# Performance work log

Measured on AMD Instinct MI355X. Metric: run time of the kernel, lower is better.

## Reference

```python
import jax, jax.numpy as jnp
import numpy as np

B, T, D = 2, 2048, 1024
H, DH = 16, 64
WINDOW = 256
SCALE = DH ** -0.5


def setup_inputs() -> dict:
    key = jax.random.key(0)
    ks = jax.random.split(key, 5)
    x = jax.random.normal(ks[0], (B, T, D), dtype=jnp.float32)
    # Linear params (y = x @ W + b form)
    w_qkv = jax.random.normal(ks[1], (D, 3 * D), dtype=jnp.float32) * (D ** -0.5)
    b_qkv = jnp.zeros((3 * D,), dtype=jnp.float32)
    w_out = jax.random.normal(ks[2], (D, D), dtype=jnp.float32) * (D ** -0.5)
    b_out = jnp.zeros((D,), dtype=jnp.float32)
    return {"x": x, "w_qkv": w_qkv, "b_qkv": b_qkv, "w_out": w_out, "b_out": b_out}


def reference(x, w_qkv, b_qkv, w_out, b_out):
    Bs, Ts, Ds = x.shape
    qkv = x @ w_qkv + b_qkv  # [B,T,3D]
    q, k, v = jnp.split(qkv, 3, axis=-1)
    # [B,H,T,dh]
    def heads(t):
        return t.reshape(Bs, Ts, H, DH).transpose(0, 2, 1, 3)
    q, k, v = heads(q), heads(k), heads(v)
    scores = jnp.einsum('bhqd,bhkd->bhqk', q, k) * SCALE
    i = jnp.arange(Ts)[:, None]
    j = jnp.arange(Ts)[None, :]
    # allowed: i - WINDOW <= j <= i  (causal + local window)
    allowed = (j <= i) & (j >= i - WINDOW)
    scores = jnp.where(allowed, scores, -jnp.inf)
    attn = jax.nn.softmax(scores, axis=-1)  # dropout is identity in eval
    out = jnp.einsum('bhqk,bhkd->bhqd', attn, v)
    out = out.transpose(0, 2, 1, 3).reshape(Bs, Ts, Ds)
    return out @ w_out + b_out
```

## Files before the change

kernel.cpp:

```cpp
#include <hip/hip_runtime.h>

#define BN 2
#define T_DIM 2048
#define D_DIM 1024
#define H_N 16
#define DH_N 64
#define WIN 256
#define NROWS (BN * T_DIM)
#define KDIM 1024

typedef __attribute__((ext_vector_type(8))) short bf16x8;
typedef __attribute__((ext_vector_type(4))) float f32x4;
typedef __attribute__((ext_vector_type(8))) unsigned short ushort8;
typedef __attribute__((ext_vector_type(4))) unsigned short u16x4;

static __device__ __forceinline__ unsigned short f2bf(float f) {
  unsigned int u = __float_as_uint(f);
  unsigned int r = (u + 0x7FFFu + ((u >> 16) & 1u)) >> 16;
  return (unsigned short)r;
}

static __device__ __forceinline__ void gl_lds16(const void* g, void* l) {
  __builtin_amdgcn_global_load_lds(
      (const __attribute__((address_space(1))) unsigned int*)g,
      (__attribute__((address_space(3))) unsigned int*)l, 16, 0, 0);
}

#define MFMA16(a, b, c) __builtin_amdgcn_mfma_f32_16x16x32_bf16(a, b, c, 0, 0, 0)

__global__ __launch_bounds__(256) void convert_bf(const float* __restrict__ src,
                                                  unsigned short* __restrict__ dst) {
  int i = (blockIdx.x * 256 + threadIdx.x) * 8;
  float4 a = *(const float4*)(src + i);
  float4 b = *(const float4*)(src + i + 4);
  ushort8 o;
  o[0] = f2bf(a.x); o[1] = f2bf(a.y); o[2] = f2bf(a.z); o[3] = f2bf(a.w);
  o[4] = f2bf(b.x); o[5] = f2bf(b.y); o[6] = f2bf(b.z); o[7] = f2bf(b.w);
  *(ushort8*)(dst + i) = o;
}

__global__ __launch_bounds__(256) void convert_t(const float* __restrict__ src,
                                                 unsigned short* __restrict__ dst,
                                                 int R, int C) {
  __shared__ float tile[64][65];
  const int t = threadIdx.x;
  const int bc = blockIdx.x * 64, br = blockIdx.y * 64;
#pragma unroll
  for (int i = 0; i < 16; ++i) {
    int idx = i * 256 + t;
    int r = idx >> 6, c = idx & 63;
    tile[r][c] = src[(size_t)(br + r) * C + bc + c];
  }
  __syncthreads();
#pragma unroll
  for (int i = 0; i < 16; ++i) {
    int idx = i * 256 + t;
    int r = idx >> 6, c = idx & 63;
    dst[(size_t)(bc + r) * R + br + c] = f2bf(tile[c][r]);
  }
}

__global__ __launch_bounds__(512) void gemm_qkv_8p(
    const unsigned short* __restrict__ A, const unsigned short* __restrict__ Bt,
    const float* __restrict__ bias, unsigned short* __restrict__ qo,
    unsigned short* __restrict__ ko, unsigned short* __restrict__ vto) {
  __shared__ unsigned short As[2][256 * 64];
  __shared__ unsigned short Bs[2][192 * 64];

  const int tid = threadIdx.x;
  const int w = tid >> 6, l = tid & 63;
  const int wr = w >> 2, wc = w & 3;
  const int l15 = l & 15, kslc = l >> 4;

  const int id = blockIdx.x;
  const int wg = (id & 7) * 32 + (id >> 3);
  const int bx = wg & 15, by = wg >> 4;
  const int r0 = by * 256, c0 = bx * 192;

  const unsigned short* Ag = A + (size_t)r0 * KDIM;
  const unsigned short* Bg = Bt + (size_t)c0 * KDIM;

  f32x4 acc[8][3];
#pragma unroll
  for (int i = 0; i < 8; ++i)
#pragma unroll
    for (int j = 0; j < 3; ++j) acc[i][j] = (f32x4){0.f, 0.f, 0.f, 0.f};

  const int grow = tid >> 3;
  const int gcol = (tid & 7) ^ (grow & 7);

#define STAGE_A(T, BUF, CH)                                                    \
  gl_lds16(Ag + (size_t)((CH)*64 + grow) * KDIM + (T)*64 + gcol * 8,           \
           (char*)&As[BUF][0] + (CH)*8192 + w * 1024)
#define STAGE_B(T, BUF, CH)                                                    \
  gl_lds16(Bg + (size_t)((CH)*64 + grow) * KDIM + (T)*64 + gcol * 8,           \
           (char*)&Bs[BUF][0] + (CH)*8192 + w * 1024)

#define LDA(CB, mi, ks)                                                        \
  (*(const bf16x8*)((const char*)&As[CB][0] +                                  \
                    (wr * 128 + (mi)*16 + l15) * 128 +                         \
                    ((((ks)*4 + kslc) ^ (l15 & 7)) << 4)))
#define LDB(CB, ni, ks)                                                        \
  (*(const bf16x8*)((const char*)&Bs[CB][0] +                                  \
                    (wc * 48 + (ni)*16 + l15) * 128 +                          \
                    ((((ks)*4 + kslc) ^ (l15 & 7)) << 4)))

#define CLUSTER12(B_, A0, A1, A2, A3, B0, B1, B2)                              \
  do {                                                                         \
    __builtin_amdgcn_s_setprio(1);                                             \
    acc[B_ + 0][0] = MFMA16(A0, B0, acc[B_ + 0][0]);                           \
    acc[B_ + 0][1] = MFMA16(A0, B1, acc[B_ + 0][1]);                           \
    acc[B_ + 0][2] = MFMA16(A0, B2, acc[B_ + 0][2]);                           \
    acc[B_ + 1][0] = MFMA16(A1, B0, acc[B_ + 1][0]);                           \
    acc[B_ + 1][1] = MFMA16(A1, B1, acc[B_ + 1][1]);                           \
    acc[B_ + 1][2] = MFMA16(A1, B2, acc[B_ + 1][2]);                           \
    acc[B_ + 2][0] = MFMA16(A2, B0, acc[B_ + 2][0]);                           \
    acc[B_ + 2][1] = MFMA16(A2, B1, acc[B_ + 2][1]);                           \
    acc[B_ + 2][2] = MFMA16(A2, B2, acc[B_ + 2][2]);                           \
    acc[B_ + 3][0] = MFMA16(A3, B0, acc[B_ + 3][0]);                           \
    acc[B_ + 3][1] = MFMA16(A3, B1, acc[B_ + 3][1]);                           \
    acc[B_ + 3][2] = MFMA16(A3, B2, acc[B_ + 3][2]);                           \
    __builtin_amdgcn_s_setprio(0);                                             \
  } while (0)

  STAGE_A(0, 0, 0); STAGE_A(0, 0, 1); STAGE_A(0, 0, 2); STAGE_A(0, 0, 3);
  STAGE_B(0, 0, 0); STAGE_B(0, 0, 1); STAGE_B(0, 0, 2);

#pragma unroll 1
  for (int t = 0; t < 15; ++t) {
    const int cb = t & 1, nb = cb ^ 1;
    STAGE_A(t + 1, nb, 0); STAGE_A(t + 1, nb, 1);
    asm volatile("s_waitcnt vmcnt(2)" ::: "memory");
    __builtin_amdgcn_s_barrier();
    {
      bf16x8 a0 = LDA(cb, 0, 0), a1 = LDA(cb, 1, 0), a2 = LDA(cb, 2, 0),
             a3 = LDA(cb, 3, 0);
      bf16x8 b0 = LDB(cb, 0, 0), b1 = LDB(cb, 1, 0), b2 = LDB(cb, 2, 0);
      CLUSTER12(0, a0, a1, a2, a3, b0, b1, b2);
      __builtin_amdgcn_s_barrier();
      bf16x8 a4 = LDA(cb, 4, 0), a5 = LDA(cb, 5, 0), a6 = LDA(cb, 6, 0),
             a7 = LDA(cb, 7, 0);
      STAGE_A(t + 1, nb, 2); STAGE_A(t + 1, nb, 3);
      __builtin_amdgcn_s_barrier();
      CLUSTER12(4, a4, a5, a6, a7, b0, b1, b2);
      __builtin_amdgcn_s_barrier();
      bf16x8 c0_ = LDA(cb, 0, 1), c1_ = LDA(cb, 1, 1), c2_ = LDA(cb, 2, 1),
             c3_ = LDA(cb, 3, 1);
      bf16x8 d0 = LDB(cb, 0, 1), d1 = LDB(cb, 1, 1), d2 = LDB(cb, 2, 1);
      STAGE_B(t + 1, nb, 0); STAGE_B(t + 1, nb, 1);
      __builtin_amdgcn_s_barrier();
      CLUSTER12(0, c0_, c1_, c2_, c3_, d0, d1, d2);
      __builtin_amdgcn_s_barrier();
      bf16x8 c4 = LDA(cb, 4, 1), c5 = LDA(cb, 5, 1), c6 = LDA(cb, 6, 1),
             c7 = LDA(cb, 7, 1);
      STAGE_B(t + 1, nb, 2);
      __builtin_amdgcn_s_barrier();
      CLUSTER12(4, c4, c5, c6, c7, d0, d1, d2);
      __builtin_amdgcn_s_barrier();
    }
  }
  asm volatile("s_waitcnt vmcnt(0)" ::: "memory");
  __builtin_amdgcn_s_barrier();
  {
    bf16x8 a0 = LDA(1, 0, 0), a1 = LDA(1, 1, 0), a2 = LDA(1, 2, 0),
           a3 = LDA(1, 3, 0);
    bf16x8 b0 = LDB(1, 0, 0), b1 = LDB(1, 1, 0), b2 = LDB(1, 2, 0);
    CLUSTER12(0, a0, a1, a2, a3, b0, b1, b2);
    bf16x8 a4 = LDA(1, 4, 0), a5 = LDA(1, 5, 0), a6 = LDA(1, 6, 0),
           a7 = LDA(1, 7, 0);
    CLUSTER12(4, a4, a5, a6, a7, b0, b1, b2);
    bf16x8 c0_ = LDA(1, 0, 1), c1_ = LDA(1, 1, 1), c2_ = LDA(1, 2, 1),
           c3_ = LDA(1, 3, 1);
    bf16x8 d0 = LDB(1, 0, 1), d1 = LDB(1, 1, 1), d2 = LDB(1, 2, 1);
    CLUSTER12(0, c0_, c1_, c2_, c3_, d0, d1, d2);
    bf16x8 c4 = LDA(1, 4, 1), c5 = LDA(1, 5, 1), c6 = LDA(1, 6, 1),
           c7 = LDA(1, 7, 1);
    CLUSTER12(4, c4, c5, c6, c7, d0, d1, d2);
  }
#undef STAGE_A
#undef STAGE_B
#undef LDA
#undef LDB
#undef CLUSTER12

#pragma unroll
  for (int ni = 0; ni < 3; ++ni) {
    const int col0 = c0 + wc * 48 + ni * 16;
    const int which = col0 >> 10;
    const int h = (col0 >> 6) & 15;
    const int dh = (col0 & 63) + l15;
    const float bv = bias[col0 + l15];
#pragma unroll
    for (int mi = 0; mi < 8; ++mi) {
      int row = r0 + wr * 128 + mi * 16 + (l >> 4) * 4;
      int b_ = row >> 11, t0 = row & 2047;
      if (which == 2) {
        u16x4 pk;
#pragma unroll
        for (int j = 0; j < 4; ++j) pk[j] = f2bf(acc[mi][ni][j] + bv);
        *(u16x4*)(vto + ((size_t)(b_ * H_N + h) * DH_N + dh) * T_DIM + t0) = pk;
      } else {
        float mul = (which == 0) ? 0.125f : 1.0f;
        unsigned short* dst = (which == 0) ? qo : ko;
#pragma unroll
        for (int j = 0; j < 4; ++j)
          dst[((size_t)(b_ * H_N + h) * T_DIM + t0 + j) * DH_N + dh] =
              f2bf((acc[mi][ni][j] + bv) * mul);
      }
    }
  }
}

__global__ __launch_bounds__(256) void gemm_out_p4(
    const unsigned short* __restrict__ A, const unsigned short* __restrict__ Bt,
    const float* __restrict__ bias, float* __restrict__ fo) {
  __shared__ unsigned short As[4][4096];
  __shared__ unsigned short Bs[4][4096];

  const int tid = threadIdx.x;
  const int w = tid >> 6, l = tid & 63;
  const int wr = w >> 1, wc = w & 1;
  const int l15 = l & 15, kslc = l >> 4;

  const int id = blockIdx.x;
  const int wg = (id & 7) * 32 + (id >> 3);
  const int bx = wg & 7, by = wg >> 3;
  const int r0 = by * 128, c0 = bx * 128;

  const unsigned short* Ag = A + (size_t)r0 * KDIM;
  const unsigned short* Bg = Bt + (size_t)c0 * KDIM;

  f32x4 acc[4][4];
#pragma unroll
  for (int i = 0; i < 4; ++i)
#pragma unroll
    for (int j = 0; j < 4; ++j) acc[i][j] = (f32x4){0.f, 0.f, 0.f, 0.f};

  const int srow = l >> 2;
  const int srcslot = (l & 3) ^ ((l >> 3) & 3);

#define STAGE_O(T, BUF)                                                        \
  do {                                                                         \
    const size_t kk0 = (size_t)(T) * 32;                                       \
    gl_lds16(Ag + (size_t)(w * 16 + srow) * KDIM + kk0 + srcslot * 8,          \
             (char*)&As[BUF][0] + w * 1024);                                   \
    gl_lds16(Ag + (size_t)(64 + w * 16 + srow) * KDIM + kk0 + srcslot * 8,     \
             (char*)&As[BUF][0] + (4 + w) * 1024);                             \
    gl_lds16(Bg + (size_t)(w * 16 + srow) * KDIM + kk0 + srcslot * 8,          \
             (char*)&Bs[BUF][0] + w * 1024);                                   \
    gl_lds16(Bg + (size_t)(64 + w * 16 + srow) * KDIM + kk0 + srcslot * 8,     \
             (char*)&Bs[BUF][0] + (4 + w) * 1024);                             \
  } while (0)

#define OCOMPUTE(CB)                                                           \
  do {                                                                         \
    bf16x8 af[4], bfr[4];                                                      \
    _Pragma("unroll") for (int mi = 0; mi < 4; ++mi) {                         \
      int row = wr * 64 + mi * 16 + l15;                                       \
      af[mi] = *(const bf16x8*)((const char*)&As[CB][0] + row * 64 +           \
                                ((kslc ^ ((row >> 1) & 3)) << 4));             \
    }                                                                          \
    _Pragma("unroll") for (int ni = 0; ni < 4; ++ni) {                         \
      int row = wc * 64 + ni * 16 + l15;                                       \
      bfr[ni] = *(const bf16x8*)((const char*)&Bs[CB][0] + row * 64 +          \
                                 ((kslc ^ ((row >> 1) & 3)) << 4));            \
    }                                                                          \
    __builtin_amdgcn_s_setprio(1);                                             \
    _Pragma("unroll") for (int mi = 0; mi < 4; ++mi)                           \
        _Pragma("unroll") for (int ni = 0; ni < 4; ++ni) acc[mi][ni] =         \
            MFMA16(af[mi], bfr[ni], acc[mi][ni]);                              \
    __builtin_amdgcn_s_setprio(0);                                             \
  } while (0)

  STAGE_O(0, 0);
  STAGE_O(1, 1);

  for (int t = 0; t < 30; ++t) {
    STAGE_O(t + 2, (t + 2) & 3);
    asm volatile("s_waitcnt vmcnt(8)" ::: "memory");
    __builtin_amdgcn_s_barrier();
    OCOMPUTE(t & 3);
  }
  asm volatile("s_waitcnt vmcnt(4)" ::: "memory");
  __builtin_amdgcn_s_barrier();
  OCOMPUTE(2);
  asm volatile("s_waitcnt vmcnt(0)" ::: "memory");
  __builtin_amdgcn_s_barrier();
  OCOMPUTE(3);
#undef STAGE_O
#undef OCOMPUTE

#pragma unroll
  for (int mi = 0; mi < 4; ++mi) {
#pragma unroll
    for (int ni = 0; ni < 4; ++ni) {
      int row = r0 + wr * 64 + mi * 16 + (l >> 4) * 4;
      int col = c0 + wc * 64 + ni * 16 + l15;
      float bv = bias[col];
#pragma unroll
      for (int j = 0; j < 4; ++j)
        fo[(size_t)(row + j) * D_DIM + col] = acc[mi][ni][j] + bv;
    }
  }
}

__global__ __launch_bounds__(256) void attn_mfma(
    const unsigned short* __restrict__ qbf,
    const unsigned short* __restrict__ kbf,
    const unsigned short* __restrict__ vtbf,
    unsigned short* __restrict__ ctx) {
  __shared__ unsigned short Ks[64 * 64];
  __shared__ unsigned short Vs[64 * 64];
  const int tid = threadIdx.x;
  const int w = tid >> 6, l = tid & 63;
  const int g = l >> 4, ln = l & 15;
  const int qt = blockIdx.x & 31;
  const int bh = blockIdx.x >> 5;
  const int q0 = qt * 64;
  const int q_abs = q0 + w * 16 + ln;

  const unsigned short* kp = kbf + (size_t)bh * T_DIM * DH_N;
  const unsigned short* vtp = vtbf + (size_t)bh * DH_N * T_DIM;

  bf16x8 qf0, qf1;
  {
    const unsigned short* qp = qbf + ((size_t)bh * T_DIM + q_abs) * DH_N;
    qf0 = *(const bf16x8*)(qp + g * 8);
    qf1 = *(const bf16x8*)(qp + 32 + g * 8);
  }

  f32x4 acc_o[4];
#pragma unroll
  for (int nd = 0; nd < 4; ++nd) acc_o[nd] = (f32x4){0.f, 0.f, 0.f, 0.f};
  float m = -1e30f, lsum = 0.f;

  const int kt_lo = (q0 >= WIN) ? (q0 - WIN) : 0;
  for (int kt = kt_lo; kt <= q0; kt += 64) {
    __syncthreads();
#pragma unroll
    for (int i = 0; i < 2; ++i) {
      int chunk = i * 256 + tid;
      int row = chunk >> 3, c16 = chunk & 7;
      int sc16 = c16 ^ (row & 7);
      int kap = 32 * ((row >> 4) & 1) + 8 * ((row & 15) >> 2) + 4 * (row >> 5) +
                (row & 3);
      gl_lds16(kp + (size_t)(kt + kap) * DH_N + sc16 * 8, (char*)Ks + chunk * 16);
      gl_lds16(vtp + (size_t)row * T_DIM + kt + sc16 * 8, (char*)Vs + chunk * 16);
    }
    __syncthreads();

    f32x4 sacc[4];
#pragma unroll
    for (int nk = 0; nk < 4; ++nk) sacc[nk] = (f32x4){0.f, 0.f, 0.f, 0.f};
#pragma unroll
    for (int ks = 0; ks < 2; ++ks) {
      bf16x8 qf = ks ? qf1 : qf0;
#pragma unroll
      for (int nk = 0; nk < 4; ++nk) {
        int rrow = nk * 16 + ln;
        int c16 = ks * 4 + g;
        bf16x8 kf = *(const bf16x8*)((const char*)Ks + rrow * 128 +
                                     ((c16 ^ (rrow & 7)) * 16));
        sacc[nk] = MFMA16(kf, qf, sacc[nk]);
      }
    }

    float p[4][4];
    float tm = -1e30f;
#pragma unroll
    for (int nk = 0; nk < 4; ++nk)
#pragma unroll
      for (int j = 0; j < 4; ++j) {
        int k_abs = kt + 32 * (nk & 1) + 8 * g + 4 * (nk >> 1) + j;
        float s = sacc[nk][j];
        bool ok = (k_abs <= q_abs) && (k_abs + WIN >= q_abs);
        s = ok ? s : -1e30f;
        p[nk][j] = s;
        tm = fmaxf(tm, s);
      }
    tm = fmaxf(tm, __shfl_xor(tm, 16, 64));
    tm = fmaxf(tm, __shfl_xor(tm, 32, 64));
    float mn = fmaxf(m, tm);
    float sc = __expf(m - mn);
    float ps = 0.f;
#pragma unroll
    for (int nk = 0; nk < 4; ++nk)
#pragma unroll
      for (int j = 0; j < 4; ++j) {
        p[nk][j] = __expf(p[nk][j] - mn);
        ps += p[nk][j];
      }
    ps += __shfl_xor(ps, 16, 64);
    ps += __shfl_xor(ps, 32, 64);
    lsum = lsum * sc + ps;
    m = mn;
#pragma unroll
    for (int nd = 0; nd < 4; ++nd) {
      acc_o[nd][0] *= sc; acc_o[nd][1] *= sc;
      acc_o[nd][2] *= sc; acc_o[nd][3] *= sc;
    }

    unsigned int pk[4][2];
#pragma unroll
    for (int nk = 0; nk < 4; ++nk) {
      pk[nk][0] = (unsigned)f2bf(p[nk][0]) | ((unsigned)f2bf(p[nk][1]) << 16);
      pk[nk][1] = (unsigned)f2bf(p[nk][2]) | ((unsigned)f2bf(p[nk][3]) << 16);
    }

#pragma unroll
    for (int ks = 0; ks < 2; ++ks) {
      union { unsigned int d[4]; bf16x8 v; } pf;
      pf.d[0] = pk[ks][0];     pf.d[1] = pk[ks][1];
      pf.d[2] = pk[2 + ks][0]; pf.d[3] = pk[2 + ks][1];
#pragma unroll
      for (int nd = 0; nd < 4; ++nd) {
        int drow = nd * 16 + ln;
        int c16 = ks * 4 + g;
        bf16x8 vf = *(const bf16x8*)((const char*)Vs + drow * 128 +
                                     ((c16 ^ (drow & 7)) * 16));
        acc_o[nd] = MFMA16(vf, pf.v, acc_o[nd]);
      }
    }
  }

  float inv = 1.f / lsum;
  const int b_ = bh >> 4, h = bh & 15;
  unsigned short* op = ctx + ((size_t)b_ * T_DIM + q_abs) * D_DIM + h * DH_N;
#pragma unroll
  for (int nd = 0; nd < 4; ++nd) {
    u16x4 o;
#pragma unroll
    for (int j = 0; j < 4; ++j) o[j] = f2bf(acc_o[nd][j] * inv);
    *(u16x4*)(op + nd * 16 + g * 4) = o;
  }
}

extern "C" void kernel_launch(void* const* d_in, const int* in_sizes, int n_in,
                              void* d_out, int out_size, void* d_ws,
                              size_t ws_size, hipStream_t stream) {
  const float* x = (const float*)d_in[0];
  const float* w_qkv = (const float*)d_in[1];
  const float* b_qkv = (const float*)d_in[2];
  const float* w_out = (const float*)d_in[3];
  const float* b_out = (const float*)d_in[4];
  float* out = (float*)d_out;

  const size_t per = (size_t)BN * H_N * T_DIM * DH_N;
  unsigned short* qbf = (unsigned short*)d_ws;
  unsigned short* kbf = qbf + per;
  unsigned short* vtbf = kbf + per;
  unsigned short* xbf = vtbf + per;
  unsigned short* wqkvt = xbf + (size_t)NROWS * D_DIM;
  unsigned short* woutt = wqkvt + (size_t)3 * D_DIM * D_DIM;
  unsigned short* ctxbf = woutt + (size_t)D_DIM * D_DIM;

  convert_bf<<<dim3(NROWS * D_DIM / (256 * 8)), dim3(256), 0, stream>>>(x, xbf);
  convert_t<<<dim3(3 * D_DIM / 64, D_DIM / 64), dim3(256), 0, stream>>>(
      w_qkv, wqkvt, D_DIM, 3 * D_DIM);
  convert_t<<<dim3(D_DIM / 64, D_DIM / 64), dim3(256), 0, stream>>>(
      w_out, woutt, D_DIM, D_DIM);

  gemm_qkv_8p<<<dim3(256), dim3(512), 0, stream>>>(xbf, wqkvt, b_qkv, qbf, kbf,
                                                   vtbf);

  attn_mfma<<<dim3(BN * H_N * (T_DIM / 64)), dim3(256), 0, stream>>>(
      qbf, kbf, vtbf, ctxbf);

  gemm_out_p4<<<dim3(256), dim3(256), 0, stream>>>(ctxbf, woutt, b_out, out);
}
```

Measured before the change: 92.40 us.

## Merge conversion kernels and prefetch whole attention window into LDS upfront

Fuses the three fp32-to-bf16 conversion/transposition kernels into a single launch dispatched by block index, cutting launch overhead. The attention kernel now issues async global-to-LDS loads for all up to five K/V tiles of the window at once, then runs a single wait and barrier before computing, removing the per-tile sync-load-sync pattern. The cost is 80KB of LDS per block, which lowers occupancy on attention.

```diff
diff --git a/kernel.cpp b/kernel.cpp
--- a/kernel.cpp
+++ b/kernel.cpp
@@ -28,35 +28,46 @@
 
 #define MFMA16(a, b, c) __builtin_amdgcn_mfma_f32_16x16x32_bf16(a, b, c, 0, 0, 0)
 
-__global__ __launch_bounds__(256) void convert_bf(const float* __restrict__ src,
-                                                  unsigned short* __restrict__ dst) {
-  int i = (blockIdx.x * 256 + threadIdx.x) * 8;
-  float4 a = *(const float4*)(src + i);
-  float4 b = *(const float4*)(src + i + 4);
-  ushort8 o;
-  o[0] = f2bf(a.x); o[1] = f2bf(a.y); o[2] = f2bf(a.z); o[3] = f2bf(a.w);
-  o[4] = f2bf(b.x); o[5] = f2bf(b.y); o[6] = f2bf(b.z); o[7] = f2bf(b.w);
-  *(ushort8*)(dst + i) = o;
-}
-
-__global__ __launch_bounds__(256) void convert_t(const float* __restrict__ src,
-                                                 unsigned short* __restrict__ dst,
-                                                 int R, int C) {
-  __shared__ float tile[64][65];
+static __device__ __forceinline__ void transpose_tile(
+    const float* __restrict__ src, unsigned short* __restrict__ dst, int R,
+    int C, int bx, int by, float* tile ) {
   const int t = threadIdx.x;
-  const int bc = blockIdx.x * 64, br = blockIdx.y * 64;
+  const int bc = bx * 64, br = by * 64;
 #pragma unroll
   for (int i = 0; i < 16; ++i) {
     int idx = i * 256 + t;
     int r = idx >> 6, c = idx & 63;
-    tile[r][c] = src[(size_t)(br + r) * C + bc + c];
+    tile[r * 65 + c] = src[(size_t)(br + r) * C + bc + c];
   }
   __syncthreads();
 #pragma unroll
   for (int i = 0; i < 16; ++i) {
     int idx = i * 256 + t;
     int r = idx >> 6, c = idx & 63;
-    dst[(size_t)(bc + r) * R + br + c] = f2bf(tile[c][r]);
+    dst[(size_t)(bc + r) * R + br + c] = f2bf(tile[c * 65 + r]);
+  }
+}
+
+__global__ __launch_bounds__(256) void convert_all(
+    const float* __restrict__ x, const float* __restrict__ w_qkv,
+    const float* __restrict__ w_out, unsigned short* __restrict__ xbf,
+    unsigned short* __restrict__ wqkvt, unsigned short* __restrict__ woutt) {
+  __shared__ float tile[64 * 65];
+  const int id = blockIdx.x;
+  if (id < 2048) {
+    int i = (id * 256 + threadIdx.x) * 8;
+    float4 a = *(const float4*)(x + i);
+    float4 b = *(const float4*)(x + i + 4);
+    ushort8 o;
+    o[0] = f2bf(a.x); o[1] = f2bf(a.y); o[2] = f2bf(a.z); o[3] = f2bf(a.w);
+    o[4] = f2bf(b.x); o[5] = f2bf(b.y); o[6] = f2bf(b.z); o[7] = f2bf(b.w);
+    *(ushort8*)(xbf + i) = o;
+  } else if (id < 2816) {
+    int j = id - 2048;
+    transpose_tile(w_qkv, wqkvt, D_DIM, 3 * D_DIM, j % 48, j / 48, tile);
+  } else {
+    int j = id - 2816;
+    transpose_tile(w_out, woutt, D_DIM, D_DIM, j % 16, j / 16, tile);
   }
 }
 
@@ -304,13 +315,13 @@
   }
 }
 
-__global__ __launch_bounds__(256) void attn_mfma(
+__global__ __launch_bounds__(256) void attn_mono(
     const unsigned short* __restrict__ qbf,
     const unsigned short* __restrict__ kbf,
     const unsigned short* __restrict__ vtbf,
     unsigned short* __restrict__ ctx) {
-  __shared__ unsigned short Ks[64 * 64];
-  __shared__ unsigned short Vs[64 * 64];
+  __shared__ unsigned short Ks[5 * 4096];
+  __shared__ unsigned short Vs[5 * 4096];
   const int tid = threadIdx.x;
   const int w = tid >> 6, l = tid & 63;
   const int g = l >> 4, ln = l & 15;
@@ -329,25 +340,38 @@
     qf1 = *(const bf16x8*)(qp + 32 + g * 8);
   }
 
+#define KAP(row) \
+  (32 * (((row) >> 4) & 1) + 8 * (((row)&15) >> 2) + 4 * ((row) >> 5) + ((row)&3))
+
+  const int kt_lo = (q0 >= WIN) ? (q0 - WIN) : 0;
+  const int nt = ((q0 - kt_lo) >> 6) + 1;
+
+  for (int i = 0; i < nt; ++i) {
+    const int kt = kt_lo + i * 64;
+#pragma unroll
+    for (int i_ = 0; i_ < 2; ++i_) {
+      int chunk = i_ * 256 + tid;
+      int row = chunk >> 3, c16 = chunk & 7;
+      int sc16 = c16 ^ (row & 7);
+      int kap = KAP(row);
+      gl_lds16(kp + (size_t)(kt + kap) * DH_N + sc16 * 8,
+               (char*)Ks + i * 8192 + chunk * 16);
+      gl_lds16(vtp + (size_t)row * T_DIM + kt + sc16 * 8,
+               (char*)Vs + i * 8192 + chunk * 16);
+    }
+  }
+  asm volatile("s_waitcnt vmcnt(0)" ::: "memory");
+  __builtin_amdgcn_s_barrier();
+
   f32x4 acc_o[4];
 #pragma unroll
   for (int nd = 0; nd < 4; ++nd) acc_o[nd] = (f32x4){0.f, 0.f, 0.f, 0.f};
   float m = -1e30f, lsum = 0.f;
 
-  const int kt_lo = (q0 >= WIN) ? (q0 - WIN) : 0;
-  for (int kt = kt_lo; kt <= q0; kt += 64) {
-    __syncthreads();
-#pragma unroll
-    for (int i = 0; i < 2; ++i) {
-      int chunk = i * 256 + tid;
-      int row = chunk >> 3, c16 = chunk & 7;
-      int sc16 = c16 ^ (row & 7);
-      int kap = 32 * ((row >> 4) & 1) + 8 * ((row & 15) >> 2) + 4 * (row >> 5) +
-                (row & 3);
-      gl_lds16(kp + (size_t)(kt + kap) * DH_N + sc16 * 8, (char*)Ks + chunk * 16);
-      gl_lds16(vtp + (size_t)row * T_DIM + kt + sc16 * 8, (char*)Vs + chunk * 16);
-    }
-    __syncthreads();
+  for (int i = 0; i < nt; ++i) {
+    const int kt = kt_lo + i * 64;
+    const char* Kb = (const char*)Ks + i * 8192;
+    const char* Vb = (const char*)Vs + i * 8192;
 
     f32x4 sacc[4];
 #pragma unroll
@@ -359,8 +383,8 @@
       for (int nk = 0; nk < 4; ++nk) {
         int rrow = nk * 16 + ln;
         int c16 = ks * 4 + g;
-        bf16x8 kf = *(const bf16x8*)((const char*)Ks + rrow * 128 +
-                                     ((c16 ^ (rrow & 7)) * 16));
+        bf16x8 kf =
+            *(const bf16x8*)(Kb + rrow * 128 + ((c16 ^ (rrow & 7)) * 16));
         sacc[nk] = MFMA16(kf, qf, sacc[nk]);
       }
     }
@@ -416,12 +440,13 @@
       for (int nd = 0; nd < 4; ++nd) {
         int drow = nd * 16 + ln;
         int c16 = ks * 4 + g;
-        bf16x8 vf = *(const bf16x8*)((const char*)Vs + drow * 128 +
-                                     ((c16 ^ (drow & 7)) * 16));
+        bf16x8 vf =
+            *(const bf16x8*)(Vb + drow * 128 + ((c16 ^ (drow & 7)) * 16));
         acc_o[nd] = MFMA16(vf, pf.v, acc_o[nd]);
       }
     }
   }
+#undef KAP
 
   float inv = 1.f / lsum;
   const int b_ = bh >> 4, h = bh & 15;
@@ -454,16 +479,13 @@
   unsigned short* woutt = wqkvt + (size_t)3 * D_DIM * D_DIM;
   unsigned short* ctxbf = woutt + (size_t)D_DIM * D_DIM;
 
-  convert_bf<<<dim3(NROWS * D_DIM / (256 * 8)), dim3(256), 0, stream>>>(x, xbf);
-  convert_t<<<dim3(3 * D_DIM / 64, D_DIM / 64), dim3(256), 0, stream>>>(
-      w_qkv, wqkvt, D_DIM, 3 * D_DIM);
-  convert_t<<<dim3(D_DIM / 64, D_DIM / 64), dim3(256), 0, stream>>>(
-      w_out, woutt, D_DIM, D_DIM);
+  convert_all<<<dim3(3072), dim3(256), 0, stream>>>(x, w_qkv, w_out, xbf,
+                                                    wqkvt, woutt);
 
   gemm_qkv_8p<<<dim3(256), dim3(512), 0, stream>>>(xbf, wqkvt, b_qkv, qbf, kbf,
                                                    vtbf);
 
-  attn_mfma<<<dim3(BN * H_N * (T_DIM / 64)), dim3(256), 0, stream>>>(
+  attn_mono<<<dim3(BN * H_N * (T_DIM / 64)), dim3(256), 0, stream>>>(
       qbf, kbf, vtbf, ctxbf);
 
   gemm_out_p4<<<dim3(256), dim3(256), 0, stream>>>(ctxbf, woutt, b_out, out);
```

After: 92.28 us. No clear change (-0.1%).
